# Kernel optimization log

Measured on AMD Instinct MI355X. Metric: run time of the kernel, lower is better.

Reference implementation:

```python
import jax, jax.numpy as jnp
import numpy as np

M, C, B, T = 512, 256, 8, 32
TOPK, LAM, RHO, DLR = 8, 0.05, 0.9, 0.03
EPS, LN_EPS = 1e-12, 1e-5


def setup_inputs() -> dict:
    key = jax.random.key(0)
    ks = jax.random.split(key, 10)

    def uni(k, shape, fan_in):
        b = 1.0 / np.sqrt(fan_in)
        return jax.random.uniform(k, shape, jnp.float32, -b, b)

    return {
        "u": jax.random.normal(ks[0], (B, T, M), jnp.float32),
        "valid": jnp.ones((B, T, 1), jnp.float32),
        "base_dictionary": jax.random.normal(ks[1], (M, C), jnp.float32) * 0.02,
        "W_cu": uni(ks[2], (C, M), M),          # code_from_u (no bias)
        "W_cc": uni(ks[3], (C, C), C),          # code_from_c (no bias)
        "W_cand_u": uni(ks[4], (M * C, M), M),  # candidate_from_u
        "b_cand_u": uni(ks[5], (M * C,), M),
        "W_cand_c": uni(ks[6], (M * C, C), C),  # candidate_from_c
        "b_cand_c": uni(ks[7], (M * C,), C),
        "W_gate": uni(ks[8], (1, M + C + 1), M + C + 1),
        "b_gate": uni(ks[9], (1,), M + C + 1),
        "ln_u_g": jnp.ones((M,), jnp.float32),
        "ln_u_b": jnp.zeros((M,), jnp.float32),
        "ln_c_g": jnp.ones((C,), jnp.float32),
        "ln_c_b": jnp.zeros((C,), jnp.float32),
    }


def _layer_norm(x, g, b):
    mu = jnp.mean(x, axis=-1, keepdims=True)
    var = jnp.mean(jnp.square(x - mu), axis=-1, keepdims=True)
    return (x - mu) * jax.lax.rsqrt(var + LN_EPS) * g + b


def _normalize_dim1(x):  # F.normalize over the model_dim axis of [B, M, C]
    n = jnp.sqrt(jnp.sum(jnp.square(x), axis=1, keepdims=True))
    return x / jnp.maximum(n, EPS)


def _topk_shrink(x):  # x: [B, C]
    shrunk = jnp.sign(x) * jax.nn.relu(jnp.abs(x) - LAM)
    _, idx = jax.lax.top_k(jnp.abs(shrunk), TOPK)  # [B, TOPK]
    rows = jnp.arange(x.shape[0])[:, None]
    mask = jnp.zeros(x.shape, jnp.bool_).at[rows, idx].set(True)
    return jnp.where(mask, shrunk, jnp.zeros_like(shrunk))


def reference(u, valid, base_dictionary, W_cu, W_cc, W_cand_u, b_cand_u,
              W_cand_c, b_cand_c, W_gate, b_gate, ln_u_g, ln_u_b, ln_c_g, ln_c_b):
    Bb = u.shape[0]
    # init_state: normalized broadcast dictionary, zero codes
    D0 = _normalize_dim1(jnp.broadcast_to(base_dictionary[None], (Bb, M, C)))
    c0 = jnp.zeros((Bb, C), u.dtype)

    def step(carry, xs):
        D, c_prev = carry
        u_t, v = xs  # [B, M], [B, 1]
        # infer_code
        logits = _layer_norm(u_t, ln_u_g, ln_u_b) @ W_cu.T + \
                 _layer_norm(c_prev, ln_c_g, ln_c_b) @ W_cc.T
        a_t = _topk_shrink(logits)
        # reconstruct + residual
        u_hat = jnp.einsum("bmc,bc->bm", D, a_t)
        r = u_t - u_hat
        # condensed code with validity mask
        c_new = RHO * c_prev + (1.0 - RHO) * a_t
        c_t = v * c_new + (1.0 - v) * c_prev
        # rank-1 dictionary update + renormalize
        d_local = _normalize_dim1(D + DLR * r[:, :, None] * a_t[:, None, :])
        # reconfiguration gate + candidate dictionary
        err = jnp.linalg.norm(r, axis=-1, keepdims=True)  # [B, 1]
        gate = jax.nn.sigmoid(
            jnp.concatenate([u_t, c_t, err], axis=-1) @ W_gate.T + b_gate)  # [B, 1]
        cand = (u_t @ W_cand_u.T + b_cand_u + c_t @ W_cand_c.T + b_cand_c)
        d_cand = _normalize_dim1(cand.reshape(Bb, M, C))
        g3 = gate[:, :, None]  # [B, 1, 1]
        d_next = _normalize_dim1((1.0 - g3) * d_local + g3 * d_cand)
        v3 = v[:, :, None]
        d_next = v3 * d_next + (1.0 - v3) * D
        z_t = jnp.einsum("bmc,bc->bm", d_next, c_t)
        return (d_next, c_t), z_t

    xs = (jnp.transpose(u, (1, 0, 2)), jnp.transpose(valid, (1, 0, 2)))
    (_, _), zs = jax.lax.scan(step, (D0, c0), xs)  # zs: [T, B, M]
    return jnp.transpose(zs, (1, 0, 2))  # [B, T, M]
```

## Files before the change

### kernel.cpp

```cpp
#include <hip/hip_runtime.h>
#include <hip/hip_bf16.h>

namespace {

constexpr int Md = 512, Cd = 256, Bd = 8, Td = 32;
constexpr float kLam = 0.05f, kRho = 0.9f, kDlr = 0.03f;
constexpr float kEps = 1e-12f, kLnEps = 1e-5f;

typedef __attribute__((ext_vector_type(8))) short short8;
typedef __attribute__((ext_vector_type(4))) float float4v;

constexpr size_t SZ_WC2   = (size_t)Cd * Cd * Md * 2;
constexpr size_t SZ_CU    = (size_t)Td * Bd * Cd * Md * 2;
constexpr size_t SZ_D     = (size_t)Bd * Cd * Md * 4;
constexpr size_t SZ_S     = SZ_D;
constexpr size_t SZ_WCUT  = (size_t)Md * Cd * 4;
constexpr size_t SZ_WCCGT = (size_t)Cd * Cd * 4;
constexpr size_t SZ_LU    = (size_t)Td * Bd * Cd * 4;
constexpr size_t SZ_UB    = (size_t)Td * Bd * Md * 2;
constexpr size_t SZ_CY    = (size_t)Bd * Cd * 4;

constexpr size_t OFF_WC2   = 0;
constexpr size_t OFF_CU    = OFF_WC2 + SZ_WC2;
constexpr size_t OFF_D0    = OFF_CU + SZ_CU;
constexpr size_t OFF_D1    = OFF_D0 + SZ_D;
constexpr size_t OFF_S     = OFF_D1 + SZ_D;
constexpr size_t OFF_WCUT  = OFF_S + SZ_S;
constexpr size_t OFF_WCCGT = OFF_WCUT + SZ_WCUT;
constexpr size_t OFF_GW    = OFF_WCCGT + SZ_WCCGT;
constexpr size_t OFF_BW    = OFF_GW + 1024;
constexpr size_t OFF_LU    = OFF_BW + 1024;
constexpr size_t OFF_UB    = OFF_LU + SZ_LU;
constexpr size_t OFF_C0    = OFF_UB + SZ_UB;
constexpr size_t OFF_C1    = OFF_C0 + SZ_CY;
constexpr size_t OFF_Y0    = OFF_C1 + SZ_CY;
constexpr size_t OFF_Y1    = OFF_Y0 + SZ_CY;

__device__ __forceinline__ unsigned short f2bf(float x) {
  __hip_bfloat16 h = __float2bfloat16(x);
  return *reinterpret_cast<unsigned short*>(&h);
}

__device__ __forceinline__ float bf2float(unsigned short x) {
  unsigned int uu = ((unsigned int)x) << 16;
  return __uint_as_float(uu);
}

__device__ __forceinline__ float block_reduce_sum(float v, float* sbuf) {
  const int tid = threadIdx.x;
  #pragma unroll
  for (int o = 32; o > 0; o >>= 1) v += __shfl_down(v, o, 64);
  __syncthreads();
  if ((tid & 63) == 0) sbuf[tid >> 6] = v;
  __syncthreads();
  return sbuf[0] + sbuf[1] + sbuf[2] + sbuf[3];
}

__device__ __forceinline__ float2 block_reduce_sum2(float a, float b, float* sbuf) {
  const int tid = threadIdx.x;
  #pragma unroll
  for (int o = 32; o > 0; o >>= 1) {
    a += __shfl_down(a, o, 64);
    b += __shfl_down(b, o, 64);
  }
  __syncthreads();
  if ((tid & 63) == 0) { sbuf[tid >> 6] = a; sbuf[4 + (tid >> 6)] = b; }
  __syncthreads();
  return make_float2(sbuf[0] + sbuf[1] + sbuf[2] + sbuf[3],
                     sbuf[4] + sbuf[5] + sbuf[6] + sbuf[7]);
}

__device__ __forceinline__ void red2(float& a, float& b, float* redf) {
  const int tid = threadIdx.x;
  #pragma unroll
  for (int o = 32; o > 0; o >>= 1) {
    a += __shfl_down(a, o, 64);
    b += __shfl_down(b, o, 64);
  }
  __syncthreads();
  if ((tid & 63) == 0) { int w = tid >> 6; redf[w * 2] = a; redf[w * 2 + 1] = b; }
  __syncthreads();
  a = redf[0] + redf[2] + redf[4] + redf[6];
  b = redf[1] + redf[3] + redf[5] + redf[7];
}

__device__ __forceinline__ void red4(float& a, float& b, float& c, float& d,
                                     float* redf) {
  const int tid = threadIdx.x;
  #pragma unroll
  for (int o = 32; o > 0; o >>= 1) {
    a += __shfl_down(a, o, 64); b += __shfl_down(b, o, 64);
    c += __shfl_down(c, o, 64); d += __shfl_down(d, o, 64);
  }
  __syncthreads();
  if ((tid & 63) == 0) {
    int w = tid >> 6;
    redf[w * 4] = a; redf[w * 4 + 1] = b; redf[w * 4 + 2] = c; redf[w * 4 + 3] = d;
  }
  __syncthreads();
  a = redf[0] + redf[4] + redf[8]  + redf[12];
  b = redf[1] + redf[5] + redf[9]  + redf[13];
  c = redf[2] + redf[6] + redf[10] + redf[14];
  d = redf[3] + redf[7] + redf[11] + redf[15];
}

__global__ __launch_bounds__(256) void k_init(const float* __restrict__ base,
                                              float* __restrict__ D1,
                                              float* __restrict__ S,
                                              float* __restrict__ c0g,
                                              float* __restrict__ y0g) {
  __shared__ float red[8];
  const int tid = threadIdx.x;
  const int c = blockIdx.x;
  float b0 = base[(size_t)tid * Cd + c];
  float b1 = base[(size_t)(tid + 256) * Cd + c];
  float ss = block_reduce_sum(b0 * b0 + b1 * b1, red);
  float rinv = 1.0f / fmaxf(sqrtf(ss), kEps);
  #pragma unroll
  for (int bb = 0; bb < Bd; ++bb) {
    size_t off = ((size_t)(bb * Cd + c)) * Md;
    D1[off + tid] = b0 * rinv;
    D1[off + tid + 256] = b1 * rinv;
  }
  size_t s0 = (size_t)c * 4096;
  #pragma unroll
  for (int k = 0; k < 16; ++k) S[s0 + k * 256 + tid] = 0.0f;
  if (c < Bd) { c0g[c * Cd + tid] = 0.0f; y0g[c * Cd + tid] = 0.0f; }
}

__global__ __launch_bounds__(256) void k_transpose_wcu(const float* __restrict__ Wcu,
                                                       float* __restrict__ WcuT) {
  int g = blockIdx.x * 256 + threadIdx.x;
  int d = g >> 8, c = g & 255;
  WcuT[g] = Wcu[(size_t)c * Md + d];
}

__global__ __launch_bounds__(256) void k_prep_wcc(const float* __restrict__ Wcc,
                                                  const float* __restrict__ lcg,
                                                  const float* __restrict__ lcb,
                                                  float* __restrict__ WccGT,
                                                  float* __restrict__ GW,
                                                  float* __restrict__ BW) {
  __shared__ float red[8];
  const int cp = blockIdx.x;
  const int tid = threadIdx.x;
  float wv = Wcc[(size_t)cp * Cd + tid];
  float g = lcg[tid], bb = lcb[tid];
  WccGT[(size_t)tid * Cd + cp] = g * wv;
  float2 ss = block_reduce_sum2(g * wv, bb * wv, red);
  if (tid == 0) { GW[cp] = ss.x; BW[cp] = ss.y; }
}

__global__ __launch_bounds__(256) void k_prep_lu(const float* __restrict__ u,
                                                 const float* __restrict__ WcuT,
                                                 const float* __restrict__ lug,
                                                 const float* __restrict__ lub,
                                                 float* __restrict__ Lu) {
  __shared__ float ln[512];
  __shared__ float red[8];
  const int n = blockIdx.x;
  const int t = n >> 3, b = n & 7;
  const int tid = threadIdx.x;
  const float* up = u + ((size_t)(b * Td + t)) * Md;
  float u0 = up[tid], u1 = up[tid + 256];
  float2 ss = block_reduce_sum2(u0 + u1, u0 * u0 + u1 * u1, red);
  float mu = ss.x * (1.0f / 512.0f);
  float var = ss.y * (1.0f / 512.0f) - mu * mu;
  float rsu = rsqrtf(var + kLnEps);
  ln[tid] = (u0 - mu) * rsu * lug[tid] + lub[tid];
  ln[tid + 256] = (u1 - mu) * rsu * lug[tid + 256] + lub[tid + 256];
  __syncthreads();
  float acc = 0.0f;
  #pragma unroll 8
  for (int i = 0; i < 512; ++i) acc = fmaf(ln[i], WcuT[(size_t)i * Cd + tid], acc);
  Lu[(size_t)n * Cd + tid] = acc;
}

__global__ __launch_bounds__(256) void k_build_wc2(const float* __restrict__ Wc,
                                                   __hip_bfloat16* __restrict__ Wc2) {
  __shared__ float tile[64][65];
  const int tid = threadIdx.x;
  const int bid = blockIdx.x;
  const int ct = bid & 3;
  const int mt = (bid >> 2) & 7;
  const int c = bid >> 5;
  const int c0p = ct * 64, m0 = mt * 64;
  const int x = tid & 63, y = tid >> 6;
  #pragma unroll
  for (int i = 0; i < 16; ++i) {
    int mm = m0 + y + i * 4;
    tile[y + i * 4][x] = Wc[((size_t)(mm * Cd + c)) * Cd + c0p + x];
  }
  __syncthreads();
  #pragma unroll
  for (int i = 0; i < 16; ++i) {
    int cp = c0p + y + i * 4;
    Wc2[((size_t)(cp * Cd + c)) * Md + m0 + x] = __float2bfloat16(tile[x][y + i * 4]);
  }
}

__global__ __launch_bounds__(256) void k_prep_u(const float* __restrict__ u,
                                                __hip_bfloat16* __restrict__ Ub) {
  const int n = blockIdx.x;
  const int t = n >> 3, b = n & 7;
  const int tid = threadIdx.x;
  const float* src = u + ((size_t)(b * Td + t)) * Md;
  __hip_bfloat16* dst = Ub + (size_t)n * Md;
  dst[tid] = __float2bfloat16(src[tid]);
  dst[tid + 256] = __float2bfloat16(src[tid + 256]);
}

__global__ __launch_bounds__(256) void k_build_cu(const float* __restrict__ Wu,
                                                  const float* __restrict__ bu,
                                                  const float* __restrict__ bc,
                                                  const __hip_bfloat16* __restrict__ Ub,
                                                  __hip_bfloat16* __restrict__ CU) {
  __shared__ unsigned short smem[256 * 72];
  const int tid = threadIdx.x;
  const int c = blockIdx.x >> 3;
  const int mt = blockIdx.x & 7;
  const int w = tid >> 6;
  const int lane = tid & 63;
  const int l15 = lane & 15;
  const int quad = lane >> 4;

  float4v acc[16];
  #pragma unroll
  for (int j = 0; j < 16; ++j) acc[j] = (float4v){0.f, 0.f, 0.f, 0.f};

  const int mrow = mt * 64 + w * 16 + l15;
  const float* Arow = Wu + ((size_t)mrow * Cd + c) * Md;
  const unsigned short* ubp = (const unsigned short*)Ub + (size_t)tid * Md;

  for (int ch = 0; ch < 16; ++ch) {
    const int d0 = ch * 32;
    short8 s0 = *(const short8*)(ubp + d0);
    short8 s1 = *(const short8*)(ubp + d0 + 8);
    short8 s2 = *(const short8*)(ubp + d0 + 16);
    short8 s3 = *(const short8*)(ubp + d0 + 24);
    __syncthreads();
    *(short8*)&smem[tid * 40 + 0]  = s0;
    *(short8*)&smem[tid * 40 + 8]  = s1;
    *(short8*)&smem[tid * 40 + 16] = s2;
    *(short8*)&smem[tid * 40 + 24] = s3;
    float4 a0 = *(const float4*)(Arow + d0 + quad * 8);
    float4 a1 = *(const float4*)(Arow + d0 + quad * 8 + 4);
    short8 af;
    af[0] = (short)f2bf(a0.x); af[1] = (short)f2bf(a0.y);
    af[2] = (short)f2bf(a0.z); af[3] = (short)f2bf(a0.w);
    af[4] = (short)f2bf(a1.x); af[5] = (short)f2bf(a1.y);
    af[6] = (short)f2bf(a1.z); af[7] = (short)f2bf(a1.w);
    __syncthreads();
    #pragma unroll
    for (int j = 0; j < 16; ++j) {
      short8 bf = *(const short8*)&smem[(j * 16 + l15) * 40 + quad * 8];
      acc[j] = __builtin_amdgcn_mfma_f32_16x16x32_bf16(af, bf, acc[j], 0, 0, 0);
    }
  }

  float bias[4];
  #pragma unroll
  for (int r2 = 0; r2 < 4; ++r2) {
    int m = mt * 64 + w * 16 + quad * 4 + r2;
    bias[r2] = bu[(size_t)m * Cd + c] + bc[(size_t)m * Cd + c];
  }
  __syncthreads();
  #pragma unroll
  for (int j = 0; j < 16; ++j) {
    int tok = j * 16 + l15;
    int mlb = w * 16 + quad * 4;
    uint2 pk;
    pk.x = (unsigned)f2bf(acc[j][0] + bias[0]) |
           ((unsigned)f2bf(acc[j][1] + bias[1]) << 16);
    pk.y = (unsigned)f2bf(acc[j][2] + bias[2]) |
           ((unsigned)f2bf(acc[j][3] + bias[3]) << 16);
    *(uint2*)&smem[tok * 72 + mlb] = pk;
  }
  __syncthreads();
  #pragma unroll
  for (int rr = 0; rr < 8; ++rr) {
    int tok = (tid >> 3) + rr * 32;
    int ml0 = (tid & 7) * 8;
    short8 vv = *(const short8*)&smem[tok * 72 + ml0];
    *(short8*)((unsigned short*)CU + ((size_t)tok * Cd + c) * Md + mt * 64 + ml0) = vv;
  }
}

__global__ __launch_bounds__(256, 4) void k_step(
    const float* __restrict__ u, const float* __restrict__ valid,
    const float* __restrict__ Wg, const float* __restrict__ bg,
    const float* __restrict__ Lu, const float* __restrict__ GW,
    const float* __restrict__ BW, const float* __restrict__ WccGT,
    const unsigned short* __restrict__ Wc2, const unsigned short* __restrict__ CUb,
    const float* __restrict__ Dprev, float* __restrict__ Dcur,
    float* __restrict__ Sg,
    const float* __restrict__ cprev, float* __restrict__ ccur,
    const float* __restrict__ Yprev, float* __restrict__ Ycur,
    float* __restrict__ out, int t) {
  __shared__ float cs[256];
  __shared__ float scs[256];
  __shared__ float shs[256];
  __shared__ float zred[256];
  __shared__ float redf[16];
  __shared__ float aval_s[8];
  __shared__ int aidx_s[8];

  const int tid = threadIdx.x;
  const int blk = blockIdx.x;
  const int b = blk >> 7;
  const int j = blk & 127;
  const int c0 = 2 * j, c1 = 2 * j + 1;

  const float cv = cprev[b * Cd + tid];
  cs[tid] = cv;
  float Yv = Yprev[b * Cd + tid];
  __syncthreads();

  if (j < 16 && t > 0) {
    const int ml = tid & 31, cgp = tid >> 5;
    const int m = j * 32 + ml;
    float acc = 0.f;
    #pragma unroll 4
    for (int i = 0; i < 32; ++i) {
      int cc = cgp * 32 + i;
      acc = fmaf(Dprev[((size_t)(b * Cd + cc)) * Md + m], cs[cc], acc);
    }
    zred[tid] = acc;
    __syncthreads();
    if (tid < 32) {
      float s = 0.f;
      #pragma unroll
      for (int g2 = 0; g2 < 8; ++g2) s += zred[g2 * 32 + tid];
      out[((size_t)(b * Td + (t - 1))) * Md + j * 32 + tid] = s;
    }
  }

  const float v = valid[b * Td + t];
  const float lam_b = v * kRho + (1.f - v);
  const float mu_b  = v * (1.f - kRho);

  float sa = cv, sb = cv * cv;
  red2(sa, sb, redf);
  float muc = sa * (1.f / 256.f);
  float rsc = rsqrtf(sb * (1.f / 256.f) - muc * muc + kLnEps);

  float lg = Lu[((size_t)(t * Bd + b)) * Cd + tid] + rsc * (Yv - muc * GW[tid]) + BW[tid];
  float sv = fmaxf(fabsf(lg) - kLam, 0.f);
  scs[tid] = sv;
  shs[tid] = (lg >= 0.f) ? sv : -sv;
  __syncthreads();

  if (tid < 64) {
    float v4[4]; int i4[4];
    #pragma unroll
    for (int k = 0; k < 4; ++k) { i4[k] = tid * 4 + k; v4[k] = scs[tid * 4 + k]; }
    for (int i = 0; i < 8; ++i) {
      float bv = v4[0]; int bi = i4[0];
      #pragma unroll
      for (int k = 1; k < 4; ++k)
        if (v4[k] > bv || (v4[k] == bv && i4[k] < bi)) { bv = v4[k]; bi = i4[k]; }
      #pragma unroll
      for (int o = 32; o > 0; o >>= 1) {
        float ov = __shfl_xor(bv, o, 64);
        int oi = __shfl_xor(bi, o, 64);
        if (ov > bv || (ov == bv && oi < bi)) { bv = ov; bi = oi; }
      }
      if (tid == 0) { aidx_s[i] = bi; aval_s[i] = shs[bi]; }
      if ((bi >> 2) == tid) v4[bi & 3] = -1.0f;
    }
  }
  __syncthreads();

  float a_t = 0.f;
  #pragma unroll
  for (int k = 0; k < 8; ++k) if (aidx_s[k] == tid) a_t = aval_s[k];
  float ct = lam_b * cv + mu_b * a_t;
  float yn = lam_b * Yv;
  #pragma unroll
  for (int k = 0; k < 8; ++k)
    yn = fmaf(mu_b * aval_s[k], WccGT[(size_t)aidx_s[k] * Cd + tid], yn);
  if (j == 0) { ccur[b * Cd + tid] = ct; Ycur[b * Cd + tid] = yn; }

  float2 uu = *(const float2*)&u[((size_t)(b * Td + t)) * Md + 2 * tid];
  float uh0 = 0.f, uh1 = 0.f;
  #pragma unroll
  for (int k = 0; k < 8; ++k) {
    float2 dp = *(const float2*)&Dprev[((size_t)(b * Cd + aidx_s[k])) * Md + 2 * tid];
    uh0 = fmaf(aval_s[k], dp.x, uh0);
    uh1 = fmaf(aval_s[k], dp.y, uh1);
  }
  float r0 = uu.x - uh0, r1 = uu.y - uh1;
  float e2 = r0 * r0 + r1 * r1;
  float gp = Wg[2 * tid] * uu.x + Wg[2 * tid + 1] * uu.y + Wg[512 + tid] * ct;
  red2(e2, gp, redf);
  float gate = 1.f / (1.f + expf(-(gp + Wg[768] * sqrtf(e2) + bg[0])));

  float a0 = 0.f, a1 = 0.f;
  #pragma unroll
  for (int k = 0; k < 8; ++k) {
    if (aidx_s[k] == c0) a0 = aval_s[k];
    if (aidx_s[k] == c1) a1 = aval_s[k];
  }
  float w0x = 0.f, w0y = 0.f, w1x = 0.f, w1y = 0.f;
  #pragma unroll
  for (int k = 0; k < 8; ++k) {
    const unsigned short* wr = Wc2 + ((size_t)aidx_s[k] * Cd) * Md;
    float av = aval_s[k];
    ushort2 q0 = *(const ushort2*)(wr + (size_t)c0 * Md + 2 * tid);
    ushort2 q1 = *(const ushort2*)(wr + (size_t)c1 * Md + 2 * tid);
    w0x = fmaf(av, bf2float(q0.x), w0x);
    w0y = fmaf(av, bf2float(q0.y), w0y);
    w1x = fmaf(av, bf2float(q1.x), w1x);
    w1y = fmaf(av, bf2float(q1.y), w1y);
  }
  float2 s0 = *(const float2*)&Sg[((size_t)(b * Cd + c0)) * Md + 2 * tid];
  float2 s1 = *(const float2*)&Sg[((size_t)(b * Cd + c1)) * Md + 2 * tid];
  float s0x = lam_b * s0.x + mu_b * w0x;
  float s0y = lam_b * s0.y + mu_b * w0y;
  float s1x = lam_b * s1.x + mu_b * w1x;
  float s1y = lam_b * s1.y + mu_b * w1y;
  *(float2*)&Sg[((size_t)(b * Cd + c0)) * Md + 2 * tid] = make_float2(s0x, s0y);
  *(float2*)&Sg[((size_t)(b * Cd + c1)) * Md + 2 * tid] = make_float2(s1x, s1y);

  const unsigned short* cup = CUb + ((size_t)((t * Bd + b) * Cd)) * Md;
  ushort2 qc0 = *(const ushort2*)(cup + (size_t)c0 * Md + 2 * tid);
  ushort2 qc1 = *(const ushort2*)(cup + (size_t)c1 * Md + 2 * tid);
  float cn0x = bf2float(qc0.x) + s0x, cn0y = bf2float(qc0.y) + s0y;
  float cn1x = bf2float(qc1.x) + s1x, cn1y = bf2float(qc1.y) + s1y;

  float2 dp0 = *(const float2*)&Dprev[((size_t)(b * Cd + c0)) * Md + 2 * tid];
  float2 dp1 = *(const float2*)&Dprev[((size_t)(b * Cd + c1)) * Md + 2 * tid];
  float dl0x = fmaf(kDlr * a0, r0, dp0.x), dl0y = fmaf(kDlr * a0, r1, dp0.y);
  float dl1x = fmaf(kDlr * a1, r0, dp1.x), dl1y = fmaf(kDlr * a1, r1, dp1.y);

  float na = cn0x * cn0x + cn0y * cn0y;
  float nb = dl0x * dl0x + dl0y * dl0y;
  float nc = cn1x * cn1x + cn1y * cn1y;
  float nd = dl1x * dl1x + dl1y * dl1y;
  red4(na, nb, nc, nd, redf);
  float ric0 = 1.f / fmaxf(sqrtf(na), kEps);
  float rid0 = 1.f / fmaxf(sqrtf(nb), kEps);
  float ric1 = 1.f / fmaxf(sqrtf(nc), kEps);
  float rid1 = 1.f / fmaxf(sqrtf(nd), kEps);

  float og = 1.f - gate;
  float e0x = og * dl0x * rid0 + gate * cn0x * ric0;
  float e0y = og * dl0y * rid0 + gate * cn0y * ric0;
  float e1x = og * dl1x * rid1 + gate * cn1x * ric1;
  float e1y = og * dl1y * rid1 + gate * cn1y * ric1;

  float q0s = e0x * e0x + e0y * e0y;
  float q1s = e1x * e1x + e1y * e1y;
  red2(q0s, q1s, redf);
  float rie0 = 1.f / fmaxf(sqrtf(q0s), kEps);
  float rie1 = 1.f / fmaxf(sqrtf(q1s), kEps);

  float ov = 1.f - v;
  float dn0x = v * (e0x * rie0) + ov * dp0.x;
  float dn0y = v * (e0y * rie0) + ov * dp0.y;
  float dn1x = v * (e1x * rie1) + ov * dp1.x;
  float dn1y = v * (e1y * rie1) + ov * dp1.y;

  *(float2*)&Dcur[((size_t)(b * Cd + c0)) * Md + 2 * tid] = make_float2(dn0x, dn0y);
  *(float2*)&Dcur[((size_t)(b * Cd + c1)) * Md + 2 * tid] = make_float2(dn1x, dn1y);
}

__global__ __launch_bounds__(256) void k_zfinal(const float* __restrict__ Dlast,
                                                const float* __restrict__ clast,
                                                float* __restrict__ out) {
  __shared__ float cs[256];
  __shared__ float zred[256];
  const int tid = threadIdx.x;
  const int b = blockIdx.x >> 4;
  const int j = blockIdx.x & 15;
  cs[tid] = clast[b * Cd + tid];
  __syncthreads();
  const int ml = tid & 31, cgp = tid >> 5;
  const int m = j * 32 + ml;
  float acc = 0.f;
  #pragma unroll 4
  for (int i = 0; i < 32; ++i) {
    int cc = cgp * 32 + i;
    acc = fmaf(Dlast[((size_t)(b * Cd + cc)) * Md + m], cs[cc], acc);
  }
  zred[tid] = acc;
  __syncthreads();
  if (tid < 32) {
// ... 23 lines not shown
  const float* bg    = (const float*)d_in[10];
  const float* lug   = (const float*)d_in[11];
  const float* lub   = (const float*)d_in[12];
  const float* lcg   = (const float*)d_in[13];
  const float* lcb   = (const float*)d_in[14];
  float* out = (float*)d_out;
  char* ws = (char*)d_ws;

  __hip_bfloat16* Wc2 = (__hip_bfloat16*)(ws + OFF_WC2);
  __hip_bfloat16* CU  = (__hip_bfloat16*)(ws + OFF_CU);
  float* Db0   = (float*)(ws + OFF_D0);
  float* Db1   = (float*)(ws + OFF_D1);
  float* Sg    = (float*)(ws + OFF_S);
  float* WcuT  = (float*)(ws + OFF_WCUT);
  float* WccGT = (float*)(ws + OFF_WCCGT);
  float* GW    = (float*)(ws + OFF_GW);
  float* BW    = (float*)(ws + OFF_BW);
  float* Lu    = (float*)(ws + OFF_LU);
  __hip_bfloat16* Ub = (__hip_bfloat16*)(ws + OFF_UB);
  float* cst0  = (float*)(ws + OFF_C0);
  float* cst1  = (float*)(ws + OFF_C1);
  float* Yg0   = (float*)(ws + OFF_Y0);
  float* Yg1   = (float*)(ws + OFF_Y1);

  hipLaunchKernelGGL(k_init, dim3(Cd), dim3(256), 0, stream, base, Db1, Sg, cst0, Yg0);
  hipLaunchKernelGGL(k_transpose_wcu, dim3(512), dim3(256), 0, stream, Wcu, WcuT);
  hipLaunchKernelGGL(k_prep_wcc, dim3(Cd), dim3(256), 0, stream,
                     Wcc, lcg, lcb, WccGT, GW, BW);
  hipLaunchKernelGGL(k_build_wc2, dim3(8192), dim3(256), 0, stream, Wc, Wc2);
  hipLaunchKernelGGL(k_prep_u, dim3(256), dim3(256), 0, stream, u, Ub);
  hipLaunchKernelGGL(k_build_cu, dim3(2048), dim3(256), 0, stream, Wu, bu, bc, Ub, CU);
  hipLaunchKernelGGL(k_prep_lu, dim3(256), dim3(256), 0, stream, u, WcuT, lug, lub, Lu);

  const unsigned short* Wc2u = (const unsigned short*)Wc2;
  const unsigned short* CUu  = (const unsigned short*)CU;

  for (int t = 0; t < Td; ++t) {
    const float* Dp = (t & 1) ? Db0 : Db1;
    float* Dc       = (t & 1) ? Db1 : Db0;
    const float* cp = (t & 1) ? cst1 : cst0;
    float* cc       = (t & 1) ? cst0 : cst1;
    const float* Yp = (t & 1) ? Yg1 : Yg0;
    float* Yc       = (t & 1) ? Yg0 : Yg1;
    hipLaunchKernelGGL(k_step, dim3(1024), dim3(256), 0, stream,
                       u, valid, Wg, bg, Lu, GW, BW, WccGT, Wc2u, CUu,
                       Dp, Dc, Sg, cp, cc, Yp, Yc, out, t);
  }
  hipLaunchKernelGGL(k_zfinal, dim3(128), dim3(256), 0, stream, Db1, cst0, out);
}
```

Baseline: 1.132 ms.

## Merge setup kernels and remap step kernel to one column per block-half with scalar-stat carry

Seven setup kernels are collapsed into two launches that dispatch on block index, cutting launch overhead and serialization between independent prep stages. The per-step kernel is reorganized so each thread handles four contiguous model elements of one column, using float4 loads and fewer block reductions (a six-way and a two-way reduction instead of several). It also carries per-batch running sum and sum-of-squares statistics in small ping-pong buffers instead of recomputing them, probably removing a reduction over the code vector each step. Risks include larger shared-memory footprint in the merged setup kernel and correctness of the new statistic recurrence.

```diff
diff --git a/kernel.cpp b/kernel.cpp
--- a/kernel.cpp
+++ b/kernel.cpp
@@ -35,6 +35,8 @@
 constexpr size_t OFF_C1    = OFF_C0 + SZ_CY;
 constexpr size_t OFF_Y0    = OFF_C1 + SZ_CY;
 constexpr size_t OFF_Y1    = OFF_Y0 + SZ_CY;
+constexpr size_t OFF_ST0   = OFF_Y1 + SZ_CY;
+constexpr size_t OFF_ST1   = OFF_ST0 + 64;
 
 __device__ __forceinline__ unsigned short f2bf(float x) {
   __hip_bfloat16 h = __float2bfloat16(x);
@@ -70,219 +72,211 @@
                      sbuf[4] + sbuf[5] + sbuf[6] + sbuf[7]);
 }
 
-__device__ __forceinline__ void red2(float& a, float& b, float* redf) {
+__device__ __forceinline__ void red6_256(float& a, float& b, float& c,
+                                         float& d, float& e, float& f,
+                                         float* rf) {
+  const int tid = threadIdx.x;
+  #pragma unroll
+  for (int o = 32; o > 0; o >>= 1) {
+    a += __shfl_down(a, o, 64); b += __shfl_down(b, o, 64);
+    c += __shfl_down(c, o, 64); d += __shfl_down(d, o, 64);
+    e += __shfl_down(e, o, 64); f += __shfl_down(f, o, 64);
+  }
+  if ((tid & 63) == 0) {
+    int w = tid >> 6;
+    rf[w * 6 + 0] = a; rf[w * 6 + 1] = b; rf[w * 6 + 2] = c;
+    rf[w * 6 + 3] = d; rf[w * 6 + 4] = e; rf[w * 6 + 5] = f;
+  }
+  __syncthreads();
+  a = rf[0] + rf[6]  + rf[12] + rf[18];
+  b = rf[1] + rf[7]  + rf[13] + rf[19];
+  c = rf[2] + rf[8]  + rf[14] + rf[20];
+  d = rf[3] + rf[9]  + rf[15] + rf[21];
+  e = rf[4] + rf[10] + rf[16] + rf[22];
+  f = rf[5] + rf[11] + rf[17] + rf[23];
+}
+
+__device__ __forceinline__ void red2_256b(float& a, float& b, float* rf) {
   const int tid = threadIdx.x;
   #pragma unroll
   for (int o = 32; o > 0; o >>= 1) {
     a += __shfl_down(a, o, 64);
     b += __shfl_down(b, o, 64);
   }
-  __syncthreads();
-  if ((tid & 63) == 0) { int w = tid >> 6; redf[w * 2] = a; redf[w * 2 + 1] = b; }
-  __syncthreads();
-  a = redf[0] + redf[2] + redf[4] + redf[6];
-  b = redf[1] + redf[3] + redf[5] + redf[7];
-}
-
-__device__ __forceinline__ void red4(float& a, float& b, float& c, float& d,
-                                     float* redf) {
-  const int tid = threadIdx.x;
-  #pragma unroll
-  for (int o = 32; o > 0; o >>= 1) {
-    a += __shfl_down(a, o, 64); b += __shfl_down(b, o, 64);
-    c += __shfl_down(c, o, 64); d += __shfl_down(d, o, 64);
-  }
-  __syncthreads();
-  if ((tid & 63) == 0) {
-    int w = tid >> 6;
-    redf[w * 4] = a; redf[w * 4 + 1] = b; redf[w * 4 + 2] = c; redf[w * 4 + 3] = d;
-  }
-  __syncthreads();
-  a = redf[0] + redf[4] + redf[8]  + redf[12];
-  b = redf[1] + redf[5] + redf[9]  + redf[13];
-  c = redf[2] + redf[6] + redf[10] + redf[14];
-  d = redf[3] + redf[7] + redf[11] + redf[15];
-}
-
-__global__ __launch_bounds__(256) void k_init(const float* __restrict__ base,
-                                              float* __restrict__ D1,
-                                              float* __restrict__ S,
-                                              float* __restrict__ c0g,
-                                              float* __restrict__ y0g) {
+  if ((tid & 63) == 0) { int w = tid >> 6; rf[w * 2] = a; rf[w * 2 + 1] = b; }
+  __syncthreads();
+  a = rf[0] + rf[2] + rf[4] + rf[6];
+  b = rf[1] + rf[3] + rf[5] + rf[7];
+}
+
+__global__ __launch_bounds__(256) void k_setup1(
+    const float* __restrict__ base, const float* __restrict__ Wcu,
+    const float* __restrict__ Wcc, const float* __restrict__ lcg,
+    const float* __restrict__ lcb, const float* __restrict__ u,
+    float* __restrict__ D1, float* __restrict__ S,
+    float* __restrict__ c0g, float* __restrict__ y0g,
+    float* __restrict__ st0, float* __restrict__ st1,
+    float* __restrict__ WcuT, float* __restrict__ WccGT,
+    float* __restrict__ GW, float* __restrict__ BW,
+    __hip_bfloat16* __restrict__ Ub) {
   __shared__ float red[8];
   const int tid = threadIdx.x;
-  const int c = blockIdx.x;
-  float b0 = base[(size_t)tid * Cd + c];
-  float b1 = base[(size_t)(tid + 256) * Cd + c];
-  float ss = block_reduce_sum(b0 * b0 + b1 * b1, red);
-  float rinv = 1.0f / fmaxf(sqrtf(ss), kEps);
-  #pragma unroll
-  for (int bb = 0; bb < Bd; ++bb) {
-    size_t off = ((size_t)(bb * Cd + c)) * Md;
-    D1[off + tid] = b0 * rinv;
-    D1[off + tid + 256] = b1 * rinv;
-  }
-  size_t s0 = (size_t)c * 4096;
-  #pragma unroll
-  for (int k = 0; k < 16; ++k) S[s0 + k * 256 + tid] = 0.0f;
-  if (c < Bd) { c0g[c * Cd + tid] = 0.0f; y0g[c * Cd + tid] = 0.0f; }
-}
-
-__global__ __launch_bounds__(256) void k_transpose_wcu(const float* __restrict__ Wcu,
-                                                       float* __restrict__ WcuT) {
-  int g = blockIdx.x * 256 + threadIdx.x;
-  int d = g >> 8, c = g & 255;
-  WcuT[g] = Wcu[(size_t)c * Md + d];
-}
-
-__global__ __launch_bounds__(256) void k_prep_wcc(const float* __restrict__ Wcc,
-                                                  const float* __restrict__ lcg,
-                                                  const float* __restrict__ lcb,
-                                                  float* __restrict__ WccGT,
-                                                  float* __restrict__ GW,
-                                                  float* __restrict__ BW) {
-  __shared__ float red[8];
-  const int cp = blockIdx.x;
-  const int tid = threadIdx.x;
-  float wv = Wcc[(size_t)cp * Cd + tid];
-  float g = lcg[tid], bb = lcb[tid];
-  WccGT[(size_t)tid * Cd + cp] = g * wv;
-  float2 ss = block_reduce_sum2(g * wv, bb * wv, red);
-  if (tid == 0) { GW[cp] = ss.x; BW[cp] = ss.y; }
-}
-
-__global__ __launch_bounds__(256) void k_prep_lu(const float* __restrict__ u,
-                                                 const float* __restrict__ WcuT,
-                                                 const float* __restrict__ lug,
-                                                 const float* __restrict__ lub,
-                                                 float* __restrict__ Lu) {
-  __shared__ float ln[512];
-  __shared__ float red[8];
-  const int n = blockIdx.x;
-  const int t = n >> 3, b = n & 7;
-  const int tid = threadIdx.x;
-  const float* up = u + ((size_t)(b * Td + t)) * Md;
-  float u0 = up[tid], u1 = up[tid + 256];
-  float2 ss = block_reduce_sum2(u0 + u1, u0 * u0 + u1 * u1, red);
-  float mu = ss.x * (1.0f / 512.0f);
-  float var = ss.y * (1.0f / 512.0f) - mu * mu;
-  float rsu = rsqrtf(var + kLnEps);
-  ln[tid] = (u0 - mu) * rsu * lug[tid] + lub[tid];
-  ln[tid + 256] = (u1 - mu) * rsu * lug[tid + 256] + lub[tid + 256];
-  __syncthreads();
-  float acc = 0.0f;
-  #pragma unroll 8
-  for (int i = 0; i < 512; ++i) acc = fmaf(ln[i], WcuT[(size_t)i * Cd + tid], acc);
-  Lu[(size_t)n * Cd + tid] = acc;
-}
-
-__global__ __launch_bounds__(256) void k_build_wc2(const float* __restrict__ Wc,
-                                                   __hip_bfloat16* __restrict__ Wc2) {
-  __shared__ float tile[64][65];
-  const int tid = threadIdx.x;
   const int bid = blockIdx.x;
-  const int ct = bid & 3;
-  const int mt = (bid >> 2) & 7;
-  const int c = bid >> 5;
-  const int c0p = ct * 64, m0 = mt * 64;
-  const int x = tid & 63, y = tid >> 6;
-  #pragma unroll
-  for (int i = 0; i < 16; ++i) {
-    int mm = m0 + y + i * 4;
-    tile[y + i * 4][x] = Wc[((size_t)(mm * Cd + c)) * Cd + c0p + x];
-  }
-  __syncthreads();
-  #pragma unroll
-  for (int i = 0; i < 16; ++i) {
-    int cp = c0p + y + i * 4;
-    Wc2[((size_t)(cp * Cd + c)) * Md + m0 + x] = __float2bfloat16(tile[x][y + i * 4]);
-  }
-}
-
-__global__ __launch_bounds__(256) void k_prep_u(const float* __restrict__ u,
-                                                __hip_bfloat16* __restrict__ Ub) {
-  const int n = blockIdx.x;
-  const int t = n >> 3, b = n & 7;
-  const int tid = threadIdx.x;
-  const float* src = u + ((size_t)(b * Td + t)) * Md;
-  __hip_bfloat16* dst = Ub + (size_t)n * Md;
-  dst[tid] = __float2bfloat16(src[tid]);
-  dst[tid + 256] = __float2bfloat16(src[tid + 256]);
-}
-
-__global__ __launch_bounds__(256) void k_build_cu(const float* __restrict__ Wu,
-                                                  const float* __restrict__ bu,
-                                                  const float* __restrict__ bc,
-                                                  const __hip_bfloat16* __restrict__ Ub,
-                                                  __hip_bfloat16* __restrict__ CU) {
-  __shared__ unsigned short smem[256 * 72];
-  const int tid = threadIdx.x;
-  const int c = blockIdx.x >> 3;
-  const int mt = blockIdx.x & 7;
-  const int w = tid >> 6;
-  const int lane = tid & 63;
-  const int l15 = lane & 15;
-  const int quad = lane >> 4;
-
-  float4v acc[16];
-  #pragma unroll
-  for (int j = 0; j < 16; ++j) acc[j] = (float4v){0.f, 0.f, 0.f, 0.f};
-
-  const int mrow = mt * 64 + w * 16 + l15;
-  const float* Arow = Wu + ((size_t)mrow * Cd + c) * Md;
-  const unsigned short* ubp = (const unsigned short*)Ub + (size_t)tid * Md;
-
-  for (int ch = 0; ch < 16; ++ch) {
-    const int d0 = ch * 32;
-    short8 s0 = *(const short8*)(ubp + d0);
-    short8 s1 = *(const short8*)(ubp + d0 + 8);
-    short8 s2 = *(const short8*)(ubp + d0 + 16);
-    short8 s3 = *(const short8*)(ubp + d0 + 24);
+  if (bid < 256) {
+    const int c = bid;
+    float b0 = base[(size_t)tid * Cd + c];
+    float b1 = base[(size_t)(tid + 256) * Cd + c];
+    float ss = block_reduce_sum(b0 * b0 + b1 * b1, red);
+    float rinv = 1.0f / fmaxf(sqrtf(ss), kEps);
+    #pragma unroll
+    for (int bb = 0; bb < Bd; ++bb) {
+      size_t off = ((size_t)(bb * Cd + c)) * Md;
+      D1[off + tid] = b0 * rinv;
+      D1[off + tid + 256] = b1 * rinv;
+    }
+    size_t s0 = (size_t)c * 4096;
+    #pragma unroll
+    for (int k = 0; k < 16; ++k) S[s0 + k * 256 + tid] = 0.0f;
+    if (c < Bd) { c0g[c * Cd + tid] = 0.0f; y0g[c * Cd + tid] = 0.0f; }
+    if (c == 0 && tid < 16) { st0[tid] = 0.0f; st1[tid] = 0.0f; }
+  } else if (bid < 768) {
+    int g = (bid - 256) * 256 + tid;
+    int d = g >> 8, c = g & 255;
+    WcuT[g] = Wcu[(size_t)c * Md + d];
+  } else if (bid < 1024) {
+    const int cp = bid - 768;
+    float wv = Wcc[(size_t)cp * Cd + tid];
+    float g = lcg[tid], bb = lcb[tid];
+    WccGT[(size_t)tid * Cd + cp] = g * wv;
+    float2 ss = block_reduce_sum2(g * wv, bb * wv, red);
+    if (tid == 0) { GW[cp] = ss.x; BW[cp] = ss.y; }
+  } else {
+    const int n = bid - 1024;
+    const int t = n >> 3, b = n & 7;
+    const float* src = u + ((size_t)(b * Td + t)) * Md;
+    __hip_bfloat16* dst = Ub + (size_t)n * Md;
+    dst[tid] = __float2bfloat16(src[tid]);
+    dst[tid + 256] = __float2bfloat16(src[tid + 256]);
+  }
+}
+
+__global__ __launch_bounds__(256) void k_setup2(
+    const float* __restrict__ Wc, const float* __restrict__ Wu,
+    const float* __restrict__ bu, const float* __restrict__ bc,
+    const __hip_bfloat16* __restrict__ Ub, const float* __restrict__ u,
+    const float* __restrict__ WcuT, const float* __restrict__ lug,
+    const float* __restrict__ lub,
+    __hip_bfloat16* __restrict__ Wc2, __hip_bfloat16* __restrict__ CU,
+    float* __restrict__ Lu) {
+  __shared__ __align__(16) char sm[256 * 72 * 2];
+  const int tid = threadIdx.x;
+  const int bid = blockIdx.x;
+  if (bid < 8192) {
+    float (*tile)[65] = (float(*)[65])sm;
+    const int ct = bid & 3;
+    const int mt = (bid >> 2) & 7;
+    const int c = bid >> 5;
+    const int c0p = ct * 64, m0 = mt * 64;
+    const int x = tid & 63, y = tid >> 6;
+    #pragma unroll
+    for (int i = 0; i < 16; ++i) {
+      int mm = m0 + y + i * 4;
+      tile[y + i * 4][x] = Wc[((size_t)(mm * Cd + c)) * Cd + c0p + x];
+    }
     __syncthreads();
-    *(short8*)&smem[tid * 40 + 0]  = s0;
-    *(short8*)&smem[tid * 40 + 8]  = s1;
-    *(short8*)&smem[tid * 40 + 16] = s2;
-    *(short8*)&smem[tid * 40 + 24] = s3;
-    float4 a0 = *(const float4*)(Arow + d0 + quad * 8);
-    float4 a1 = *(const float4*)(Arow + d0 + quad * 8 + 4);
-    short8 af;
-    af[0] = (short)f2bf(a0.x); af[1] = (short)f2bf(a0.y);
-    af[2] = (short)f2bf(a0.z); af[3] = (short)f2bf(a0.w);
-    af[4] = (short)f2bf(a1.x); af[5] = (short)f2bf(a1.y);
-    af[6] = (short)f2bf(a1.z); af[7] = (short)f2bf(a1.w);
+    #pragma unroll
+    for (int i = 0; i < 16; ++i) {
+      int cp = c0p + y + i * 4;
+      Wc2[((size_t)(cp * Cd + c)) * Md + m0 + x] = __float2bfloat16(tile[x][y + i * 4]);
+    }
+  } else if (bid < 10240) {
+    unsigned short* smem = (unsigned short*)sm;
+    const int bb = bid - 8192;
+    const int c = bb >> 3;
+    const int mt = bb & 7;
+    const int w = tid >> 6;
+    const int lane = tid & 63;
+    const int l15 = lane & 15;
+    const int quad = lane >> 4;
+
+    float4v acc[16];
+    #pragma unroll
+    for (int j = 0; j < 16; ++j) acc[j] = (float4v){0.f, 0.f, 0.f, 0.f};
+
+    const int mrow = mt * 64 + w * 16 + l15;
+    const float* Arow = Wu + ((size_t)mrow * Cd + c) * Md;
+    const unsigned short* ubp = (const unsigned short*)Ub + (size_t)tid * Md;
+
+    for (int ch = 0; ch < 16; ++ch) {
+      const int d0 = ch * 32;
+      short8 s0 = *(const short8*)(ubp + d0);
+      short8 s1 = *(const short8*)(ubp + d0 + 8);
+      short8 s2 = *(const short8*)(ubp + d0 + 16);
+      short8 s3 = *(const short8*)(ubp + d0 + 24);
+      __syncthreads();
+      *(short8*)&smem[tid * 40 + 0]  = s0;
+      *(short8*)&smem[tid * 40 + 8]  = s1;
+      *(short8*)&smem[tid * 40 + 16] = s2;
+      *(short8*)&smem[tid * 40 + 24] = s3;
+      float4 a0 = *(const float4*)(Arow + d0 + quad * 8);
+      float4 a1 = *(const float4*)(Arow + d0 + quad * 8 + 4);
+      short8 af;
+      af[0] = (short)f2bf(a0.x); af[1] = (short)f2bf(a0.y);
+      af[2] = (short)f2bf(a0.z); af[3] = (short)f2bf(a0.w);
+      af[4] = (short)f2bf(a1.x); af[5] = (short)f2bf(a1.y);
+      af[6] = (short)f2bf(a1.z); af[7] = (short)f2bf(a1.w);
+      __syncthreads();
+      #pragma unroll
+      for (int j = 0; j < 16; ++j) {
+        short8 bf = *(const short8*)&smem[(j * 16 + l15) * 40 + quad * 8];
+        acc[j] = __builtin_amdgcn_mfma_f32_16x16x32_bf16(af, bf, acc[j], 0, 0, 0);
+      }
+    }
+
+    float bias[4];
+    #pragma unroll
+    for (int r2 = 0; r2 < 4; ++r2) {
+      int m = mt * 64 + w * 16 + quad * 4 + r2;
+      bias[r2] = bu[(size_t)m * Cd + c] + bc[(size_t)m * Cd + c];
+    }
     __syncthreads();
     #pragma unroll
     for (int j = 0; j < 16; ++j) {
-      short8 bf = *(const short8*)&smem[(j * 16 + l15) * 40 + quad * 8];
-      acc[j] = __builtin_amdgcn_mfma_f32_16x16x32_bf16(af, bf, acc[j], 0, 0, 0);
-    }
-  }
-
-  float bias[4];
-  #pragma unroll
-  for (int r2 = 0; r2 < 4; ++r2) {
-    int m = mt * 64 + w * 16 + quad * 4 + r2;
-    bias[r2] = bu[(size_t)m * Cd + c] + bc[(size_t)m * Cd + c];
-  }
-  __syncthreads();
-  #pragma unroll
-  for (int j = 0; j < 16; ++j) {
-    int tok = j * 16 + l15;
-    int mlb = w * 16 + quad * 4;
-    uint2 pk;
-    pk.x = (unsigned)f2bf(acc[j][0] + bias[0]) |
-           ((unsigned)f2bf(acc[j][1] + bias[1]) << 16);
-    pk.y = (unsigned)f2bf(acc[j][2] + bias[2]) |
-           ((unsigned)f2bf(acc[j][3] + bias[3]) << 16);
-    *(uint2*)&smem[tok * 72 + mlb] = pk;
-  }
-  __syncthreads();
-  #pragma unroll
-  for (int rr = 0; rr < 8; ++rr) {
-    int tok = (tid >> 3) + rr * 32;
-    int ml0 = (tid & 7) * 8;
-    short8 vv = *(const short8*)&smem[tok * 72 + ml0];
-    *(short8*)((unsigned short*)CU + ((size_t)tok * Cd + c) * Md + mt * 64 + ml0) = vv;
+      int tok = j * 16 + l15;
+      int mlb = w * 16 + quad * 4;
+      uint2 pk;
+      pk.x = (unsigned)f2bf(acc[j][0] + bias[0]) |
+             ((unsigned)f2bf(acc[j][1] + bias[1]) << 16);
+      pk.y = (unsigned)f2bf(acc[j][2] + bias[2]) |
+             ((unsigned)f2bf(acc[j][3] + bias[3]) << 16);
+      *(uint2*)&smem[tok * 72 + mlb] = pk;
+    }
+    __syncthreads();
+    #pragma unroll
+    for (int rr = 0; rr < 8; ++rr) {
+      int tok = (tid >> 3) + rr * 32;
+      int ml0 = (tid & 7) * 8;
+      short8 vv = *(const short8*)&smem[tok * 72 + ml0];
+      *(short8*)((unsigned short*)CU + ((size_t)tok * Cd + c) * Md + mt * 64 + ml0) = vv;
+    }
+  } else {
+    float* ln = (float*)sm;
+    float* red = ln + 512;
+    const int n = bid - 10240;
+    const int t = n >> 3, b = n & 7;
+    const float* up = u + ((size_t)(b * Td + t)) * Md;
+    float u0 = up[tid], u1 = up[tid + 256];
+    float2 ss = block_reduce_sum2(u0 + u1, u0 * u0 + u1 * u1, red);
+    float mu = ss.x * (1.0f / 512.0f);
+    float var = ss.y * (1.0f / 512.0f) - mu * mu;
+    float rsu = rsqrtf(var + kLnEps);
+    ln[tid] = (u0 - mu) * rsu * lug[tid] + lub[tid];
+    ln[tid + 256] = (u1 - mu) * rsu * lug[tid + 256] + lub[tid + 256];
+    __syncthreads();
+    float acc = 0.0f;
+    #pragma unroll 8
+    for (int i = 0; i < 512; ++i) acc = fmaf(ln[i], WcuT[(size_t)i * Cd + tid], acc);
+    Lu[(size_t)n * Cd + tid] = acc;
   }
 }
 
@@ -296,173 +290,172 @@
     float* __restrict__ Sg,
     const float* __restrict__ cprev, float* __restrict__ ccur,
     const float* __restrict__ Yprev, float* __restrict__ Ycur,
+    const float* __restrict__ STp, float* __restrict__ STc,
     float* __restrict__ out, int t) {
-  __shared__ float cs[256];
   __shared__ float scs[256];
   __shared__ float shs[256];
   __shared__ float zred[256];
-  __shared__ float redf[16];
-  __shared__ float aval_s[8];
-  __shared__ int aidx_s[8];
+  __shared__ float redf[32];
 
   const int tid = threadIdx.x;
   const int blk = blockIdx.x;
   const int b = blk >> 7;
   const int j = blk & 127;
-  const int c0 = 2 * j, c1 = 2 * j + 1;
+  const int grp = tid >> 7;
+  const int col = 2 * j + grp;
+  const int mb = (tid & 127) * 4;
 
   const float cv = cprev[b * Cd + tid];
-  cs[tid] = cv;
-  float Yv = Yprev[b * Cd + tid];
-  __syncthreads();
-
-  if (j < 16 && t > 0) {
-    const int ml = tid & 31, cgp = tid >> 5;
+  const float Yv = Yprev[b * Cd + tid];
+  const float Ssum = STp[b * 2], Ssq = STp[b * 2 + 1];
+  const float lu = Lu[((size_t)(t * Bd + b)) * Cd + tid];
+  const float gw = GW[tid], bw = BW[tid];
+  const float v = valid[b * Td + t];
+  const float4 uu = *(const float4*)&u[((size_t)(b * Td + t)) * Md + mb];
+  const float4 Sv = *(const float4*)&Sg[((size_t)(b * Cd + col)) * Md + mb];
+  const float4 dp = *(const float4*)&Dprev[((size_t)(b * Cd + col)) * Md + mb];
+  const ushort4 cuq =
+      *(const ushort4*)&CUb[((size_t)((t * Bd + b) * Cd + col)) * Md + mb];
+
+  const float lam_b = v * kRho + (1.f - v);
+  const float mu_b  = v * (1.f - kRho);
+
+  float zacc = 0.f;
+  const bool zb = (j < 16) && (t > 0);
+  if (zb) {
+    const int ml = tid & 31, cg2 = tid >> 5;
     const int m = j * 32 + ml;
-    float acc = 0.f;
     #pragma unroll 4
     for (int i = 0; i < 32; ++i) {
-      int cc = cgp * 32 + i;
-      acc = fmaf(Dprev[((size_t)(b * Cd + cc)) * Md + m], cs[cc], acc);
-    }
-    zred[tid] = acc;
-    __syncthreads();
-    if (tid < 32) {
-      float s = 0.f;
-      #pragma unroll
-      for (int g2 = 0; g2 < 8; ++g2) s += zred[g2 * 32 + tid];
-      out[((size_t)(b * Td + (t - 1))) * Md + j * 32 + tid] = s;
-    }
-  }
-
-  const float v = valid[b * Td + t];
-  const float lam_b = v * kRho + (1.f - v);
-  const float mu_b  = v * (1.f - kRho);
-
-  float sa = cv, sb = cv * cv;
-  red2(sa, sb, redf);
-  float muc = sa * (1.f / 256.f);
-  float rsc = rsqrtf(sb * (1.f / 256.f) - muc * muc + kLnEps);
-
-  float lg = Lu[((size_t)(t * Bd + b)) * Cd + tid] + rsc * (Yv - muc * GW[tid]) + BW[tid];
+      int cc = cg2 * 32 + i;
+      zacc = fmaf(Dprev[((size_t)(b * Cd + cc)) * Md + m], cprev[b * Cd + cc], zacc);
+    }
+  }
+
+  const float muc = Ssum * (1.f / 256.f);
+  const float rsc = rsqrtf(Ssq * (1.f / 256.f) - muc * muc + kLnEps);
+  float lg = lu + rsc * (Yv - muc * gw) + bw;
   float sv = fmaxf(fabsf(lg) - kLam, 0.f);
   scs[tid] = sv;
   shs[tid] = (lg >= 0.f) ? sv : -sv;
-  __syncthreads();
-
-  if (tid < 64) {
-    float v4[4]; int i4[4];
-    #pragma unroll
-    for (int k = 0; k < 4; ++k) { i4[k] = tid * 4 + k; v4[k] = scs[tid * 4 + k]; }
-    for (int i = 0; i < 8; ++i) {
-      float bv = v4[0]; int bi = i4[0];
-      #pragma unroll
-      for (int k = 1; k < 4; ++k)
-        if (v4[k] > bv || (v4[k] == bv && i4[k] < bi)) { bv = v4[k]; bi = i4[k]; }
-      #pragma unroll
-      for (int o = 32; o > 0; o >>= 1) {
-        float ov = __shfl_xor(bv, o, 64);
-        int oi = __shfl_xor(bi, o, 64);
-        if (ov > bv || (ov == bv && oi < bi)) { bv = ov; bi = oi; }
-      }
-      if (tid == 0) { aidx_s[i] = bi; aval_s[i] = shs[bi]; }
-      if ((bi >> 2) == tid) v4[bi & 3] = -1.0f;
-    }
-  }
-  __syncthreads();
-
-  float a_t = 0.f;
-  #pragma unroll
-  for (int k = 0; k < 8; ++k) if (aidx_s[k] == tid) a_t = aval_s[k];
+  if (zb) zred[tid] = zacc;
+  __syncthreads();
+
+  if (zb && tid < 32) {
+    float s = 0.f;
+    #pragma unroll
+    for (int g2 = 0; g2 < 8; ++g2) s += zred[g2 * 32 + tid];
+    out[((size_t)(b * Td + (t - 1))) * Md + j * 32 + tid] = s;
+  }
+
+  const int lane = tid & 63;
+  float v4[4]; int i4[4];
+  #pragma unroll
+  for (int k = 0; k < 4; ++k) { i4[k] = lane * 4 + k; v4[k] = scs[lane * 4 + k]; }
+  float av[8]; int ai[8];
+  #pragma unroll
+  for (int i = 0; i < 8; ++i) {
+    float bv = v4[0]; int bi = i4[0];
+    #pragma unroll
+    for (int k = 1; k < 4; ++k)
+      if (v4[k] > bv || (v4[k] == bv && i4[k] < bi)) { bv = v4[k]; bi = i4[k]; }
+    #pragma unroll
+    for (int o = 32; o > 0; o >>= 1) {
+      float ov2 = __shfl_xor(bv, o, 64);
+      int oi = __shfl_xor(bi, o, 64);
+      if (ov2 > bv || (ov2 == bv && oi < bi)) { bv = ov2; bi = oi; }
+    }
+    ai[i] = bi; av[i] = shs[bi];
+    if ((bi >> 2) == lane) v4[bi & 3] = -1.0f;
+  }
+
+  float a_t = 0.f, a_col = 0.f;
+  #pragma unroll
+  for (int k = 0; k < 8; ++k) {
+    if (ai[k] == tid) a_t = av[k];
+    if (ai[k] == col) a_col = av[k];
+  }
   float ct = lam_b * cv + mu_b * a_t;
   float yn = lam_b * Yv;
   #pragma unroll
   for (int k = 0; k < 8; ++k)
-    yn = fmaf(mu_b * aval_s[k], WccGT[(size_t)aidx_s[k] * Cd + tid], yn);
+    yn = fmaf(mu_b * av[k], WccGT[(size_t)ai[k] * Cd + tid], yn);
   if (j == 0) { ccur[b * Cd + tid] = ct; Ycur[b * Cd + tid] = yn; }
 
-  float2 uu = *(const float2*)&u[((size_t)(b * Td + t)) * Md + 2 * tid];
-  float uh0 = 0.f, uh1 = 0.f;
+  float uh0 = 0.f, uh1 = 0.f, uh2 = 0.f, uh3 = 0.f;
   #pragma unroll
   for (int k = 0; k < 8; ++k) {
-    float2 dp = *(const float2*)&Dprev[((size_t)(b * Cd + aidx_s[k])) * Md + 2 * tid];
-    uh0 = fmaf(aval_s[k], dp.x, uh0);
-    uh1 = fmaf(aval_s[k], dp.y, uh1);
-  }
-  float r0 = uu.x - uh0, r1 = uu.y - uh1;
-  float e2 = r0 * r0 + r1 * r1;
-  float gp = Wg[2 * tid] * uu.x + Wg[2 * tid + 1] * uu.y + Wg[512 + tid] * ct;
-  red2(e2, gp, redf);
-  float gate = 1.f / (1.f + expf(-(gp + Wg[768] * sqrtf(e2) + bg[0])));
-
-  float a0 = 0.f, a1 = 0.f;
+    float4 dq = *(const float4*)&Dprev[((size_t)(b * Cd + ai[k])) * Md + mb];
+    uh0 = fmaf(av[k], dq.x, uh0); uh1 = fmaf(av[k], dq.y, uh1);
+    uh2 = fmaf(av[k], dq.z, uh2); uh3 = fmaf(av[k], dq.w, uh3);
+  }
+  float r0 = uu.x - uh0, r1 = uu.y - uh1, r2 = uu.z - uh2, r3 = uu.w - uh3;
+
+  float w0 = 0.f, w1 = 0.f, w2 = 0.f, w3 = 0.f;
   #pragma unroll
   for (int k = 0; k < 8; ++k) {
-    if (aidx_s[k] == c0) a0 = aval_s[k];
-    if (aidx_s[k] == c1) a1 = aval_s[k];
-  }
-  float w0x = 0.f, w0y = 0.f, w1x = 0.f, w1y = 0.f;
-  #pragma unroll
-  for (int k = 0; k < 8; ++k) {
-    const unsigned short* wr = Wc2 + ((size_t)aidx_s[k] * Cd) * Md;
-    float av = aval_s[k];
-    ushort2 q0 = *(const ushort2*)(wr + (size_t)c0 * Md + 2 * tid);
-    ushort2 q1 = *(const ushort2*)(wr + (size_t)c1 * Md + 2 * tid);
-    w0x = fmaf(av, bf2float(q0.x), w0x);
-    w0y = fmaf(av, bf2float(q0.y), w0y);
-    w1x = fmaf(av, bf2float(q1.x), w1x);
-    w1y = fmaf(av, bf2float(q1.y), w1y);
-  }
-  float2 s0 = *(const float2*)&Sg[((size_t)(b * Cd + c0)) * Md + 2 * tid];
-  float2 s1 = *(const float2*)&Sg[((size_t)(b * Cd + c1)) * Md + 2 * tid];
-  float s0x = lam_b * s0.x + mu_b * w0x;
-  float s0y = lam_b * s0.y + mu_b * w0y;
-  float s1x = lam_b * s1.x + mu_b * w1x;
-  float s1y = lam_b * s1.y + mu_b * w1y;
-  *(float2*)&Sg[((size_t)(b * Cd + c0)) * Md + 2 * tid] = make_float2(s0x, s0y);
-  *(float2*)&Sg[((size_t)(b * Cd + c1)) * Md + 2 * tid] = make_float2(s1x, s1y);
-
-  const unsigned short* cup = CUb + ((size_t)((t * Bd + b) * Cd)) * Md;
-  ushort2 qc0 = *(const ushort2*)(cup + (size_t)c0 * Md + 2 * tid);
-  ushort2 qc1 = *(const ushort2*)(cup + (size_t)c1 * Md + 2 * tid);
-  float cn0x = bf2float(qc0.x) + s0x, cn0y = bf2float(qc0.y) + s0y;
-  float cn1x = bf2float(qc1.x) + s1x, cn1y = bf2float(qc1.y) + s1y;
-
-  float2 dp0 = *(const float2*)&Dprev[((size_t)(b * Cd + c0)) * Md + 2 * tid];
-  float2 dp1 = *(const float2*)&Dprev[((size_t)(b * Cd + c1)) * Md + 2 * tid];
-  float dl0x = fmaf(kDlr * a0, r0, dp0.x), dl0y = fmaf(kDlr * a0, r1, dp0.y);
-  float dl1x = fmaf(kDlr * a1, r0, dp1.x), dl1y = fmaf(kDlr * a1, r1, dp1.y);
-
-  float na = cn0x * cn0x + cn0y * cn0y;
-  float nb = dl0x * dl0x + dl0y * dl0y;
-  float nc = cn1x * cn1x + cn1y * cn1y;
-  float nd = dl1x * dl1x + dl1y * dl1y;
-  red4(na, nb, nc, nd, redf);
-  float ric0 = 1.f / fmaxf(sqrtf(na), kEps);
-  float rid0 = 1.f / fmaxf(sqrtf(nb), kEps);
-  float ric1 = 1.f / fmaxf(sqrtf(nc), kEps);
-  float rid1 = 1.f / fmaxf(sqrtf(nd), kEps);
-
+    ushort4 q = *(const ushort4*)&Wc2[((size_t)(ai[k] * Cd + col)) * Md + mb];
+    float avk = av[k];
+    w0 = fmaf(avk, bf2float(q.x), w0); w1 = fmaf(avk, bf2float(q.y), w1);
+    w2 = fmaf(avk, bf2float(q.z), w2); w3 = fmaf(avk, bf2float(q.w), w3);
+  }
+  float sn0 = lam_b * Sv.x + mu_b * w0;
+  float sn1 = lam_b * Sv.y + mu_b * w1;
+  float sn2 = lam_b * Sv.z + mu_b * w2;
+  float sn3 = lam_b * Sv.w + mu_b * w3;
+  *(float4*)&Sg[((size_t)(b * Cd + col)) * Md + mb] =
+      make_float4(sn0, sn1, sn2, sn3);
+
+  float cn0 = bf2float(cuq.x) + sn0, cn1 = bf2float(cuq.y) + sn1;
+  float cn2 = bf2float(cuq.z) + sn2, cn3 = bf2float(cuq.w) + sn3;
+  float dl0 = fmaf(kDlr * a_col, r0, dp.x), dl1 = fmaf(kDlr * a_col, r1, dp.y);
+  float dl2 = fmaf(kDlr * a_col, r2, dp.z), dl3 = fmaf(kDlr * a_col, r3, dp.w);
+
+  float candN = cn0 * cn0 + cn1 * cn1 + cn2 * cn2 + cn3 * cn3;
+  float dlN = dl0 * dl0 + dl1 * dl1 + dl2 * dl2 + dl3 * dl3;
+  float err2 = (grp == 0) ? (r0 * r0 + r1 * r1 + r2 * r2 + r3 * r3) : 0.f;
+  const float4 wg4 = *(const float4*)&Wg[mb];
+  float gpu = wg4.x * uu.x + wg4.y * uu.y + wg4.z * uu.z + wg4.w * uu.w;
+  float gp = ((grp == 0) ? gpu : 0.f) + Wg[512 + tid] * ct;
+  float na = grp ? 0.f : candN, nc = grp ? candN : 0.f;
+  float nb = grp ? 0.f : dlN,   nd = grp ? dlN : 0.f;
+  red6_256(err2, gp, na, nb, nc, nd, redf);
+
+  float gate = 1.f / (1.f + expf(-(gp + Wg[768] * sqrtf(err2) + bg[0])));
+  float ric = 1.f / fmaxf(sqrtf(grp ? nc : na), kEps);
+  float rid = 1.f / fmaxf(sqrtf(grp ? nd : nb), kEps);
   float og = 1.f - gate;
-  float e0x = og * dl0x * rid0 + gate * cn0x * ric0;
-  float e0y = og * dl0y * rid0 + gate * cn0y * ric0;
-  float e1x = og * dl1x * rid1 + gate * cn1x * ric1;
-  float e1y = og * dl1y * rid1 + gate * cn1y * ric1;
-
-  float q0s = e0x * e0x + e0y * e0y;
-  float q1s = e1x * e1x + e1y * e1y;
-  red2(q0s, q1s, redf);
-  float rie0 = 1.f / fmaxf(sqrtf(q0s), kEps);
-  float rie1 = 1.f / fmaxf(sqrtf(q1s), kEps);
+  float e0 = og * dl0 * rid + gate * cn0 * ric;
+  float e1 = og * dl1 * rid + gate * cn1 * ric;
+  float e2v = og * dl2 * rid + gate * cn2 * ric;
+  float e3 = og * dl3 * rid + gate * cn3 * ric;
+
+  float qs = e0 * e0 + e1 * e1 + e2v * e2v + e3 * e3;
+  float qa = grp ? 0.f : qs, qb = grp ? qs : 0.f;
+  red2_256b(qa, qb, redf + 24);
+  float rie = 1.f / fmaxf(sqrtf(grp ? qb : qa), kEps);
 
   float ov = 1.f - v;
-  float dn0x = v * (e0x * rie0) + ov * dp0.x;
-  float dn0y = v * (e0y * rie0) + ov * dp0.y;
-  float dn1x = v * (e1x * rie1) + ov * dp1.x;
-  float dn1y = v * (e1y * rie1) + ov * dp1.y;
-
-  *(float2*)&Dcur[((size_t)(b * Cd + c0)) * Md + 2 * tid] = make_float2(dn0x, dn0y);
-  *(float2*)&Dcur[((size_t)(b * Cd + c1)) * Md + 2 * tid] = make_float2(dn1x, dn1y);
+  float dn0 = v * (e0 * rie) + ov * dp.x;
+  float dn1 = v * (e1 * rie) + ov * dp.y;
+  float dn2 = v * (e2v * rie) + ov * dp.z;
+  float dn3 = v * (e3 * rie) + ov * dp.w;
+  *(float4*)&Dcur[((size_t)(b * Cd + col)) * Md + mb] =
+      make_float4(dn0, dn1, dn2, dn3);
+
+  if (j == 0 && tid == 0) {
+    float sA = 0.f, sCA = 0.f, sA2 = 0.f;
+    #pragma unroll
+    for (int k = 0; k < 8; ++k) {
+      float cpk = cprev[b * Cd + ai[k]];
+      sA += av[k];
+      sCA = fmaf(cpk, av[k], sCA);
+      sA2 = fmaf(av[k], av[k], sA2);
+    }
+    STc[b * 2] = lam_b * Ssum + mu_b * sA;
+    STc[b * 2 + 1] = lam_b * lam_b * Ssq + 2.f * lam_b * mu_b * sCA
+                     + mu_b * mu_b * sA2;
+  }
 }
 
 __global__ __launch_bounds__(256) void k_zfinal(const float* __restrict__ Dlast,
@@ -532,15 +525,14 @@
   float* cst1  = (float*)(ws + OFF_C1);
   float* Yg0   = (float*)(ws + OFF_Y0);
   float* Yg1   = (float*)(ws + OFF_Y1);
-
-  hipLaunchKernelGGL(k_init, dim3(Cd), dim3(256), 0, stream, base, Db1, Sg, cst0, Yg0);
-  hipLaunchKernelGGL(k_transpose_wcu, dim3(512), dim3(256), 0, stream, Wcu, WcuT);
-  hipLaunchKernelGGL(k_prep_wcc, dim3(Cd), dim3(256), 0, stream,
-                     Wcc, lcg, lcb, WccGT, GW, BW);
-  hipLaunchKernelGGL(k_build_wc2, dim3(8192), dim3(256), 0, stream, Wc, Wc2);
-  hipLaunchKernelGGL(k_prep_u, dim3(256), dim3(256), 0, stream, u, Ub);
-  hipLaunchKernelGGL(k_build_cu, dim3(2048), dim3(256), 0, stream, Wu, bu, bc, Ub, CU);
-  hipLaunchKernelGGL(k_prep_lu, dim3(256), dim3(256), 0, stream, u, WcuT, lug, lub, Lu);
+  float* ST0   = (float*)(ws + OFF_ST0);
+  float* ST1   = (float*)(ws + OFF_ST1);
+
+  hipLaunchKernelGGL(k_setup1, dim3(1280), dim3(256), 0, stream,
+                     base, Wcu, Wcc, lcg, lcb, u,
+                     Db1, Sg, cst0, Yg0, ST0, ST1, WcuT, WccGT, GW, BW, Ub);
+  hipLaunchKernelGGL(k_setup2, dim3(10496), dim3(256), 0, stream,
+                     Wc, Wu, bu, bc, Ub, u, WcuT, lug, lub, Wc2, CU, Lu);
 
   const unsigned short* Wc2u = (const unsigned short*)Wc2;
   const unsigned short* CUu  = (const unsigned short*)CU;
@@ -552,9 +544,11 @@
     float* cc       = (t & 1) ? cst0 : cst1;
     const float* Yp = (t & 1) ? Yg1 : Yg0;
     float* Yc       = (t & 1) ? Yg0 : Yg1;
+    const float* Sp = (t & 1) ? ST1 : ST0;
+    float* Sc       = (t & 1) ? ST0 : ST1;
     hipLaunchKernelGGL(k_step, dim3(1024), dim3(256), 0, stream,
                        u, valid, Wg, bg, Lu, GW, BW, WccGT, Wc2u, CUu,
-                       Dp, Dc, Sg, cp, cc, Yp, Yc, out, t);
+                       Dp, Dc, Sg, cp, cc, Yp, Yc, Sp, Sc, out, t);
   }
   hipLaunchKernelGGL(k_zfinal, dim3(128), dim3(256), 0, stream, Db1, cst0, out);
 }
```

Result: no change. 1.120 ms (-1.1%).
